# Kernel tuning notes

Measured on AMD Instinct MI355X. Metric: run time of the kernel, lower is better.

Reference implementation:

```python
import jax, jax.numpy as jnp
import numpy as np

K_CODES = 64
EPS_LN = 1e-5


def hamilton_product(p, q):
    # p, q: [..., D] with D = 4*Q, components ordered (r, i, j, k)
    Q = p.shape[-1] // 4
    pr, pi, pj, pk = (p[..., :Q], p[..., Q:2*Q], p[..., 2*Q:3*Q], p[..., 3*Q:])
    qr, qi, qj, qk = (q[..., :Q], q[..., Q:2*Q], q[..., 2*Q:3*Q], q[..., 3*Q:])
    out_r = pr * qr - pi * qi - pj * qj - pk * qk
    out_i = pr * qi + pi * qr + pj * qk - pk * qj
    out_j = pr * qj - pi * qk + pj * qr + pk * qi
    out_k = pr * qk + pi * qj - pj * qi + pk * qr
    return jnp.concatenate([out_r, out_i, out_j, out_k], axis=-1)


def quaternion_linear(x, w4, b):
    # w4: [4, Qo, Qi] stacked (r, i, j, k); builds Hamilton block matrix [D, D]
    r, i, j, k = w4[0], w4[1], w4[2], w4[3]
    W = jnp.block([[r, -i, -j, -k],
                   [i,  r, -k,  j],
                   [j,  k,  r, -i],
                   [k, -j,  i,  r]])
    return x @ W.T + b


def quaternion_layernorm(x, gamma, beta):
    # independent LayerNorm over each quaternion component (4 chunks of size Q)
    Qd = x.shape[-1] // 4
    xs = x.reshape(*x.shape[:-1], 4, Qd)
    mu = xs.mean(axis=-1, keepdims=True)
    var = ((xs - mu) ** 2).mean(axis=-1, keepdims=True)
    xn = (xs - mu) / jnp.sqrt(var + EPS_LN)
    out = xn * gamma + beta  # gamma/beta: [4, Qd]
    return out.reshape(*x.shape[:-1], 4 * Qd)


def setup_inputs() -> dict:
    key = jax.random.key(0)
    ks = jax.random.split(key, 8)
    B, N, D, m = 8, 4096, 512, 3
    Qd = D // 4
    q = jax.random.normal(ks[0], (B, N, D), dtype=jnp.float32)
    assign_idx = jax.random.randint(ks[1], (B, N, m), 0, K_CODES)
    assign_w = jax.random.uniform(ks[2], (B, N, m), dtype=jnp.float32)
    contribute_mask = jnp.ones((B, N), dtype=jnp.float32)
    scale = 0.5 / np.sqrt(Qd)
    proto_w = jax.random.normal(ks[3], (4, Qd, Qd), dtype=jnp.float32) * scale
    proto_b = jax.random.normal(ks[4], (D,), dtype=jnp.float32) * 0.01
    upd_w = jax.random.normal(ks[5], (4, Qd, Qd), dtype=jnp.float32) * scale
    upd_b = jax.random.normal(ks[6], (D,), dtype=jnp.float32) * 0.01
    ln_gamma = jnp.ones((4, Qd), dtype=jnp.float32)
    ln_beta = jnp.zeros((4, Qd), dtype=jnp.float32)
    return {"q": q, "assign_idx": assign_idx, "assign_w": assign_w,
            "contribute_mask": contribute_mask, "proto_w": proto_w,
            "proto_b": proto_b, "upd_w": upd_w, "upd_b": upd_b,
            "ln_gamma": ln_gamma, "ln_beta": ln_beta}


def reference(q, assign_idx, assign_w, contribute_mask, proto_w, proto_b,
              upd_w, upd_b, ln_gamma, ln_beta):
    B, N, D = q.shape
    m = assign_idx.shape[-1]
    K = K_CODES

    # --- scatter-add prototype aggregation ---
    agg_w = assign_w * contribute_mask[..., None]            # [B, N, m]
    flat_idx = assign_idx.reshape(B, N * m)                  # [B, N*m]
    flat_w = agg_w.reshape(B, N * m, 1)                      # [B, N*m, 1]
    weighted_q = (q[:, :, None, :] * agg_w[..., None]).reshape(B, N * m, D)

    seg = lambda v, idx: jax.ops.segment_sum(v, idx, num_segments=K)
    proto = jax.vmap(seg)(weighted_q, flat_idx)              # [B, K, D]
    weight_sum = jax.vmap(seg)(flat_w, flat_idx)             # [B, K, 1]
    proto = proto / (weight_sum + 1e-6)
    proto = quaternion_linear(proto, proto_w, proto_b)       # [B, K, D]

    # --- gather prototypes per observation + Hamilton routing ---
    proto_per_obs = jax.vmap(lambda p, idx: p[idx])(proto, assign_idx)  # [B, N, m, D]
    routed = hamilton_product(q[:, :, None, :], proto_per_obs)          # [B, N, m, D]
    msg = (routed * assign_w[..., None]).sum(axis=2)                    # [B, N, D]
    msg = quaternion_linear(msg, upd_w, upd_b)

    q_new = quaternion_layernorm(q + msg, ln_gamma, ln_beta)
    return q_new, proto
```

## Files before the change

### kernel.cpp

```cpp
#include <hip/hip_runtime.h>
#include <hip/hip_bf16.h>

#define B_ 8
#define N_ 4096
#define D_ 512
#define K_ 64
#define QD_ 128

typedef float f32x4 __attribute__((ext_vector_type(4)));
typedef short short8 __attribute__((ext_vector_type(8)));
typedef unsigned short u16;
typedef unsigned int u32;

__device__ __forceinline__ u16 f2bf(float f) {
  u32 u = __float_as_uint(f);
  return (u16)((u + 0x7fffu + ((u >> 16) & 1u)) >> 16);
}
__device__ __forceinline__ float bf2f(u16 h) {
  return __uint_as_float((u32)h << 16);
}

__device__ __forceinline__ void load8f(const float* p, float* r) {
  float4 a = *(const float4*)(p);
  float4 b = *(const float4*)(p + 4);
  r[0] = a.x; r[1] = a.y; r[2] = a.z; r[3] = a.w;
  r[4] = b.x; r[5] = b.y; r[6] = b.z; r[7] = b.w;
}

__global__ __launch_bounds__(256) void k_wexp_frag(
    const float* __restrict__ uw, const float* __restrict__ pw,
    u16* __restrict__ uwf, u16* __restrict__ pwf) {
  const int gid = blockIdx.x * 256 + threadIdx.x;
  const int sel = gid >> 18;
  const int idx = gid & ((1 << 18) - 1);
  const int e = idx & 7;
  const int lane = (idx >> 3) & 63;
  const int ks = (idx >> 9) & 15;
  const int cf = idx >> 13;
  const int col = (cf >> 3) * 128 + (cf & 7) * 16 + (lane & 15);
  const int v = ks * 32 + (lane >> 4) * 8 + e;
  const int u = col >> 7, a = col & 127, c = v >> 7, bb = v & 127;
  const int   matT[4][4] = {{0,1,2,3},{1,0,3,2},{2,3,0,1},{3,2,1,0}};
  const float sgnT[4][4] = {{1.f,-1.f,-1.f,-1.f},{1.f,1.f,-1.f,1.f},
                            {1.f,1.f,1.f,-1.f},{1.f,-1.f,1.f,1.f}};
  const float* w4 = sel ? pw : uw;
  u16* dst = sel ? pwf : uwf;
  dst[idx] = f2bf(sgnT[u][c] * w4[matT[u][c] * QD_ * QD_ + a * QD_ + bb]);
}

__global__ __launch_bounds__(256) void k_bldA(
    const int* __restrict__ aidx, const float* __restrict__ aw,
    const float* __restrict__ mask, u16* __restrict__ A) {
  const int gid = blockIdx.x * 256 + threadIdx.x;
  const int b = gid >> 12, n = gid & 4095;
  const size_t ib = (size_t)gid * 3;
  const int k0 = aidx[ib], k1 = aidx[ib + 1], k2 = aidx[ib + 2];
  const float mk = mask[gid];
  float w0 = aw[ib] * mk, w1 = aw[ib + 1] * mk, w2 = aw[ib + 2] * mk;
  bool skip1 = false, skip2 = false;
  if (k1 == k0) { w0 += w1; skip1 = true; }
  if (k2 == k0) { w0 += w2; skip2 = true; }
  else if (k2 == k1 && !skip1) { w1 += w2; skip2 = true; }
  u16* Ab = A + (size_t)b * K_ * N_;
  Ab[(size_t)k0 * N_ + n] = f2bf(w0);
  if (!skip1) Ab[(size_t)k1 * N_ + n] = f2bf(w1);
  if (!skip2) Ab[(size_t)k2 * N_ + n] = f2bf(w2);
}

__global__ __launch_bounds__(256) void k_gemmA(
    const u16* __restrict__ A, const float* __restrict__ q,
    float* __restrict__ proto_raw) {
  __shared__ __align__(16) u16 Bt[128 * 64];
  const int t = threadIdx.x;
  const int kc = blockIdx.x;
  const int dq = blockIdx.y;
  const int b = blockIdx.z;
  const int n_base = kc * 256;
  const u16* Ab = A + (size_t)b * K_ * N_;
  const float* qb = q + ((size_t)b * N_ + n_base) * D_ + dq * 128;

  const int lane = t & 63, wv = t >> 6;
  const int g = lane >> 4, l16 = lane & 15;
  const int sn = t >> 2, sdq = (t & 3) * 32;

  f32x4 acc[4][2];
#pragma unroll
  for (int mt = 0; mt < 4; ++mt)
#pragma unroll
    for (int nt = 0; nt < 2; ++nt) { f32x4 z = {0.f,0.f,0.f,0.f}; acc[mt][nt] = z; }

  float4 pre[8];
#pragma unroll
  for (int e = 0; e < 8; ++e)
    pre[e] = *(const float4*)(qb + (size_t)sn * D_ + sdq + e * 4);

  for (int sub = 0; sub < 4; ++sub) {
    __syncthreads();
#pragma unroll
    for (int e = 0; e < 8; ++e) {
      const float4 v = pre[e];
#pragma unroll
      for (int x = 0; x < 4; ++x) {
        const int d = sdq + e * 4 + x;
        const float fv = (x == 0) ? v.x : (x == 1) ? v.y : (x == 2) ? v.z : v.w;
        const int byte = (d * 128 + sn * 2) ^ ((d & 7) << 4);
        *(u16*)((char*)Bt + byte) = f2bf(fv);
      }
    }
    float4 nxt[8];
    if (sub < 3) {
#pragma unroll
      for (int e = 0; e < 8; ++e)
        nxt[e] = *(const float4*)(qb + (size_t)((sub + 1) * 64 + sn) * D_ + sdq + e * 4);
    }
    __syncthreads();
    const int n0 = n_base + sub * 64;
#pragma unroll
    for (int ks = 0; ks < 2; ++ks) {
      short8 bfrag[2];
#pragma unroll
      for (int nt = 0; nt < 2; ++nt) {
        const int d = wv * 32 + nt * 16 + l16;
        const int byte = (d * 128 + (ks * 32 + g * 8) * 2) ^ ((d & 7) << 4);
        bfrag[nt] = *(const short8*)((const char*)Bt + byte);
      }
#pragma unroll
      for (int mt = 0; mt < 4; ++mt) {
        const short8 afr = *(const short8*)(Ab + (size_t)(mt * 16 + l16) * N_ +
                                            n0 + ks * 32 + g * 8);
#pragma unroll
        for (int nt = 0; nt < 2; ++nt)
          acc[mt][nt] = __builtin_amdgcn_mfma_f32_16x16x32_bf16(afr, bfrag[nt], acc[mt][nt], 0, 0, 0);
      }
    }
#pragma unroll
    for (int e = 0; e < 8; ++e) pre[e] = nxt[e];
  }

#pragma unroll
  for (int mt = 0; mt < 4; ++mt)
#pragma unroll
    for (int nt = 0; nt < 2; ++nt)
#pragma unroll
      for (int rg = 0; rg < 4; ++rg) {
        const int code = mt * 16 + g * 4 + rg;
        const int d = dq * 128 + wv * 32 + nt * 16 + l16;
        atomicAdd(&proto_raw[((size_t)b * K_ + code) * D_ + d], acc[mt][nt][rg]);
      }
}

__global__ __launch_bounds__(64) void k_rowsum(const u16* __restrict__ A,
                                               float* __restrict__ wsum) {
  const int row = blockIdx.x;
  const int t = threadIdx.x;
  const u16* p = A + (size_t)row * N_ + t * 64;
  float s = 0.f;
#pragma unroll
  for (int i = 0; i < 8; ++i) {
    const short8 v = *(const short8*)(p + i * 8);
#pragma unroll
    for (int e = 0; e < 8; ++e) s += bf2f((u16)v[e]);
  }
  s += __shfl_xor(s, 1);  s += __shfl_xor(s, 2);  s += __shfl_xor(s, 4);
  s += __shfl_xor(s, 8);  s += __shfl_xor(s, 16); s += __shfl_xor(s, 32);
  if (t == 0) wsum[row] = s;
}

__global__ __launch_bounds__(256) void k_proto_mfma(
    const float* __restrict__ proto_raw, const float* __restrict__ wsum,
    const u16* __restrict__ pwf, const float* __restrict__ pb,
    float* __restrict__ proto_t, float* __restrict__ out_proto) {
  __shared__ __align__(16) u16 msgL[16 * 512];
  __shared__ float invs[16];
  const int t = threadIdx.x;
  const size_t R0 = (size_t)blockIdx.x * 16;
  if (t < 16) invs[t] = 1.f / (wsum[R0 + t] + 1e-6f);
  __syncthreads();

  {
    const int s = t & 15, row = t >> 4;
    const float iv = invs[row];
    const float* base = proto_raw + (R0 + row) * D_;
    const int swz = (row & 7) << 4;
#pragma unroll
    for (int u = 0; u < 4; ++u) {
      float m[8];
      load8f(base + u * 128 + s * 8, m);
      uint4 val;
      val.x = (u32)f2bf(m[0]*iv) | ((u32)f2bf(m[1]*iv) << 16);
      val.y = (u32)f2bf(m[2]*iv) | ((u32)f2bf(m[3]*iv) << 16);
      val.z = (u32)f2bf(m[4]*iv) | ((u32)f2bf(m[5]*iv) << 16);
      val.w = (u32)f2bf(m[6]*iv) | ((u32)f2bf(m[7]*iv) << 16);
      const int byte = (row * 1024 + u * 256 + s * 16) ^ swz;
      *(uint4*)((char*)msgL + byte) = val;
    }
  }
  __syncthreads();

  const int lane = t & 63, wv = t >> 6;
  const int g = lane >> 4, l16 = lane & 15;
  f32x4 acc[8];
#pragma unroll
  for (int f = 0; f < 8; ++f) { f32x4 z = {0.f,0.f,0.f,0.f}; acc[f] = z; }
#pragma unroll 4
  for (int ks = 0; ks < 16; ++ks) {
    const int arow = l16;
    const short8 a = *(const short8*)((const char*)msgL +
        ((arow * 1024 + ks * 64 + g * 16) ^ ((arow & 7) << 4)));
#pragma unroll
    for (int f = 0; f < 8; ++f) {
      const short8 bv = *(const short8*)(pwf +
          ((size_t)((wv * 8 + f) * 16 + ks) * 64 + lane) * 8);
      acc[f] = __builtin_amdgcn_mfma_f32_16x16x32_bf16(a, bv, acc[f], 0, 0, 0);
    }
  }

#pragma unroll
  for (int f = 0; f < 8; ++f) {
    const int col = wv * 128 + f * 16 + l16;
    const float pbv = pb[col];
#pragma unroll
    for (int rg = 0; rg < 4; ++rg) {
      const size_t row = R0 + g * 4 + rg;
      const float v = acc[f][rg] + pbv;
      proto_t[row * D_ + col] = v;
      out_proto[row * D_ + col] = v;
    }
  }
}

__global__ __launch_bounds__(256) void k_main7b(
    const float* __restrict__ q, const int* __restrict__ aidx,
    const float* __restrict__ aw, const float* __restrict__ proto_t,
    const u16* __restrict__ uwf, const float* __restrict__ ub,
    const float* __restrict__ gamma, const float* __restrict__ beta,
    float* __restrict__ out_q) {
  __shared__ __align__(16) u16 msgL[32 * 512];
  const int t = threadIdx.x;
  const size_t R0 = (size_t)blockIdx.x * 32;

  {
    const int s = t & 15, rowHalf = t >> 4;
    int kks[2][3]; float wws[2][3];
#pragma unroll
    for (int p = 0; p < 2; ++p) {
      const size_t gr = R0 + p * 16 + rowHalf;
      const int* ip = aidx + gr * 3;
      const float* wp = aw + gr * 3;
#pragma unroll
      for (int j = 0; j < 3; ++j) { kks[p][j] = ip[j]; wws[p][j] = wp[j]; }
    }
#pragma unroll
    for (int p = 0; p < 2; ++p) {
      const int row = p * 16 + rowHalf;
      const size_t gr = R0 + row;
      const int b = (int)(gr >> 12);
      const float* qp = q + gr * D_ + s * 8;
      float qr_[8], qi_[8], qj_[8], qk_[8];
      load8f(qp, qr_); load8f(qp + 128, qi_);
      load8f(qp + 256, qj_); load8f(qp + 384, qk_);
      float mr[8], mi[8], mj[8], mk[8];
#pragma unroll
      for (int e = 0; e < 8; ++e) { mr[e] = mi[e] = mj[e] = mk[e] = 0.f; }
#pragma unroll
      for (int j = 0; j < 3; ++j) {
        const float w = wws[p][j];
        const float* pp = proto_t + (size_t)(b * K_ + kks[p][j]) * D_ + s * 8;
        float pr[8], pi[8], pj[8], pk[8];
        load8f(pp, pr); load8f(pp + 128, pi);
        load8f(pp + 256, pj); load8f(pp + 384, pk);
#pragma unroll
        for (int e = 0; e < 8; ++e) {
          mr[e] += w * (qr_[e]*pr[e] - qi_[e]*pi[e] - qj_[e]*pj[e] - qk_[e]*pk[e]);
          mi[e] += w * (qr_[e]*pi[e] + qi_[e]*pr[e] + qj_[e]*pk[e] - qk_[e]*pj[e]);
          mj[e] += w * (qr_[e]*pj[e] - qi_[e]*pk[e] + qj_[e]*pr[e] + qk_[e]*pi[e]);
          mk[e] += w * (qr_[e]*pk[e] + qi_[e]*pj[e] - qj_[e]*pi[e] + qk_[e]*pr[e]);
        }
      }
      const int swz = (row & 7) << 4;
      const float* srcs[4] = {mr, mi, mj, mk};
#pragma unroll
      for (int u = 0; u < 4; ++u) {
        const float* m = srcs[u];
        uint4 val;
        val.x = (u32)f2bf(m[0]) | ((u32)f2bf(m[1]) << 16);
        val.y = (u32)f2bf(m[2]) | ((u32)f2bf(m[3]) << 16);
        val.z = (u32)f2bf(m[4]) | ((u32)f2bf(m[5]) << 16);
        val.w = (u32)f2bf(m[6]) | ((u32)f2bf(m[7]) << 16);
        const int byte = (row * 1024 + u * 256 + s * 16) ^ swz;
        *(uint4*)((char*)msgL + byte) = val;
      }
    }
  }
  __syncthreads();

  const int lane = t & 63, c4 = t >> 6;
  const int g = lane >> 4, l16 = lane & 15;
  f32x4 acc[2][8];
#pragma unroll
  for (int st = 0; st < 2; ++st)
#pragma unroll
    for (int f = 0; f < 8; ++f) { f32x4 z = {0.f,0.f,0.f,0.f}; acc[st][f] = z; }
#pragma unroll 2
  for (int ks = 0; ks < 16; ++ks) {
    short8 bfr[8];
#pragma unroll
    for (int f = 0; f < 8; ++f)
      bfr[f] = *(const short8*)(uwf +
          ((size_t)((c4 * 8 + f) * 16 + ks) * 64 + lane) * 8);
#pragma unroll
    for (int st = 0; st < 2; ++st) {
      const int arow = st * 16 + l16;
      const short8 a = *(const short8*)((const char*)msgL +
          ((arow * 1024 + ks * 64 + g * 16) ^ ((arow & 7) << 4)));
#pragma unroll
      for (int f = 0; f < 8; ++f)
        acc[st][f] = __builtin_amdgcn_mfma_f32_16x16x32_bf16(a, bfr[f], acc[st][f], 0, 0, 0);
    }
  }

  const int colQ = c4 * 128;
#pragma unroll
  for (int st = 0; st < 2; ++st)
#pragma unroll
    for (int f = 0; f < 8; ++f) {
      const int col = colQ + f * 16 + l16;
      const float ubv = ub[col];
#pragma unroll
      for (int rg = 0; rg < 4; ++rg) {
        const size_t row = R0 + st * 16 + g * 4 + rg;
        acc[st][f][rg] += ubv + q[row * D_ + col];
      }
    }
#pragma unroll
  for (int st = 0; st < 2; ++st)
#pragma unroll
    for (int rg = 0; rg < 4; ++rg) {
      float s = 0.f;
#pragma unroll
      for (int f = 0; f < 8; ++f) s += acc[st][f][rg];
      s += __shfl_xor(s, 1); s += __shfl_xor(s, 2);
      s += __shfl_xor(s, 4); s += __shfl_xor(s, 8);
      const float mean = s * 0.0078125f;
      float sq = 0.f;
#pragma unroll
      for (int f = 0; f < 8; ++f) {
        const float d = acc[st][f][rg] - mean; sq += d * d;
      }
      sq += __shfl_xor(sq, 1); sq += __shfl_xor(sq, 2);
      sq += __shfl_xor(sq, 4); sq += __shfl_xor(sq, 8);
      const float rstd = rsqrtf(sq * 0.0078125f + 1e-5f);
      const size_t row = R0 + st * 16 + g * 4 + rg;
#pragma unroll
      for (int f = 0; f < 8; ++f) {
        const int col = colQ + f * 16 + l16;
        const float xn = (acc[st][f][rg] - mean) * rstd;
        out_q[row * D_ + col] = xn * gamma[col] + beta[col];
      }
    }
}

extern "C" void kernel_launch(void* const* d_in, const int* in_sizes, int n_in,
                              void* d_out, int out_size, void* d_ws, size_t ws_size,
                              hipStream_t stream) {
  const float* q     = (const float*)d_in[0];
  const int*   aidx  = (const int*)d_in[1];
  const float* aw    = (const float*)d_in[2];
  const float* mask  = (const float*)d_in[3];
  const float* pw    = (const float*)d_in[4];
  const float* pb    = (const float*)d_in[5];
  const float* uw    = (const float*)d_in[6];
  const float* ub    = (const float*)d_in[7];
  const float* gamma = (const float*)d_in[8];
  const float* beta  = (const float*)d_in[9];

  char* ws = (char*)d_ws;
  const size_t MB = 1 << 20;
  float* proto_raw = (float*)ws;
  float* wsum      = (float*)(ws + MB);
  u16*   A         = (u16*)(ws + MB + 4096);
  float* proto_t   = (float*)(ws + 5 * MB + 4096);
  u16*   uwf       = (u16*)(ws + 6 * MB + 4096);
  u16*   pwf       = (u16*)(ws + 6 * MB + 4096 + (512 << 10));

  float* out_q = (float*)d_out;
  float* out_proto = out_q + (size_t)B_ * N_ * D_;

  hipMemsetAsync(ws, 0, 5 * MB + 4096, stream);
  k_wexp_frag<<<2048, 256, 0, stream>>>(uw, pw, uwf, pwf);
  k_bldA<<<128, 256, 0, stream>>>(aidx, aw, mask, A);
  k_gemmA<<<dim3(16, 4, 8), 256, 0, stream>>>(A, q, proto_raw);
  k_rowsum<<<512, 64, 0, stream>>>(A, wsum);
  k_proto_mfma<<<32, 256, 0, stream>>>(proto_raw, wsum, pwf, pb, proto_t, out_proto);
  k_main7b<<<1024, 256, 0, stream>>>(q, aidx, aw, proto_t, uwf, ub, gamma, beta, out_q);
}
```

Baseline: 138.3 us.

## Factor Hamilton product out of prototype sum, fuse rowsum into GEMM, zero A in-kernel

```diff
diff --git a/kernel.cpp b/kernel.cpp
--- a/kernel.cpp
+++ b/kernel.cpp
@@ -25,6 +25,17 @@
   float4 b = *(const float4*)(p + 4);
   r[0] = a.x; r[1] = a.y; r[2] = a.z; r[3] = a.w;
   r[4] = b.x; r[5] = b.y; r[6] = b.z; r[7] = b.w;
+}
+
+__device__ __forceinline__ void store_comp(char* msgL, int row, int u, int s,
+                                           int swz, const float* m) {
+  uint4 val;
+  val.x = (u32)f2bf(m[0]) | ((u32)f2bf(m[1]) << 16);
+  val.y = (u32)f2bf(m[2]) | ((u32)f2bf(m[3]) << 16);
+  val.z = (u32)f2bf(m[4]) | ((u32)f2bf(m[5]) << 16);
+  val.w = (u32)f2bf(m[6]) | ((u32)f2bf(m[7]) << 16);
+  const int byte = (row * 1024 + u * 256 + s * 16) ^ swz;
+  *(uint4*)(msgL + byte) = val;
 }
 
 __global__ __launch_bounds__(256) void k_wexp_frag(
@@ -62,6 +73,8 @@
   if (k2 == k0) { w0 += w2; skip2 = true; }
   else if (k2 == k1 && !skip1) { w1 += w2; skip2 = true; }
   u16* Ab = A + (size_t)b * K_ * N_;
+#pragma unroll
+  for (int k = 0; k < K_; ++k) Ab[(size_t)k * N_ + n] = 0;
   Ab[(size_t)k0 * N_ + n] = f2bf(w0);
   if (!skip1) Ab[(size_t)k1 * N_ + n] = f2bf(w1);
   if (!skip2) Ab[(size_t)k2 * N_ + n] = f2bf(w2);
@@ -69,7 +82,7 @@
 
 __global__ __launch_bounds__(256) void k_gemmA(
     const u16* __restrict__ A, const float* __restrict__ q,
-    float* __restrict__ proto_raw) {
+    float* __restrict__ proto_raw, float* __restrict__ wsum) {
   __shared__ __align__(16) u16 Bt[128 * 64];
   const int t = threadIdx.x;
   const int kc = blockIdx.x;
@@ -147,23 +160,21 @@
         const int d = dq * 128 + wv * 32 + nt * 16 + l16;
         atomicAdd(&proto_raw[((size_t)b * K_ + code) * D_ + d], acc[mt][nt][rg]);
       }
-}
-
-__global__ __launch_bounds__(64) void k_rowsum(const u16* __restrict__ A,
-                                               float* __restrict__ wsum) {
-  const int row = blockIdx.x;
-  const int t = threadIdx.x;
-  const u16* p = A + (size_t)row * N_ + t * 64;
-  float s = 0.f;
-#pragma unroll
-  for (int i = 0; i < 8; ++i) {
-    const short8 v = *(const short8*)(p + i * 8);
-#pragma unroll
-    for (int e = 0; e < 8; ++e) s += bf2f((u16)v[e]);
-  }
-  s += __shfl_xor(s, 1);  s += __shfl_xor(s, 2);  s += __shfl_xor(s, 4);
-  s += __shfl_xor(s, 8);  s += __shfl_xor(s, 16); s += __shfl_xor(s, 32);
-  if (t == 0) wsum[row] = s;
+
+  if (dq == 0) {
+    const int k = t >> 2, part = t & 3;
+    const u16* ap = Ab + (size_t)k * N_ + n_base + part * 64;
+    float s = 0.f;
+#pragma unroll
+    for (int i = 0; i < 8; ++i) {
+      const short8 v = *(const short8*)(ap + i * 8);
+#pragma unroll
+      for (int e = 0; e < 8; ++e) s += bf2f((u16)v[e]);
+    }
+    s += __shfl_xor(s, 1);
+    s += __shfl_xor(s, 2);
+    if (part == 0) atomicAdd(&wsum[b * K_ + k], s);
+  }
 }
 
 __global__ __launch_bounds__(256) void k_proto_mfma(
@@ -186,13 +197,9 @@
     for (int u = 0; u < 4; ++u) {
       float m[8];
       load8f(base + u * 128 + s * 8, m);
-      uint4 val;
-      val.x = (u32)f2bf(m[0]*iv) | ((u32)f2bf(m[1]*iv) << 16);
-      val.y = (u32)f2bf(m[2]*iv) | ((u32)f2bf(m[3]*iv) << 16);
-      val.z = (u32)f2bf(m[4]*iv) | ((u32)f2bf(m[5]*iv) << 16);
-      val.w = (u32)f2bf(m[6]*iv) | ((u32)f2bf(m[7]*iv) << 16);
-      const int byte = (row * 1024 + u * 256 + s * 16) ^ swz;
-      *(uint4*)((char*)msgL + byte) = val;
+#pragma unroll
+      for (int e = 0; e < 8; ++e) m[e] *= iv;
+      store_comp((char*)msgL, row, u, s, swz, m);
     }
   }
   __syncthreads();
@@ -229,7 +236,7 @@
   }
 }
 
-__global__ __launch_bounds__(256) void k_main7b(
+__global__ __launch_bounds__(256) void k_main8(
     const float* __restrict__ q, const int* __restrict__ aidx,
     const float* __restrict__ aw, const float* __restrict__ proto_t,
     const u16* __restrict__ uwf, const float* __restrict__ ub,
@@ -259,9 +266,9 @@
       float qr_[8], qi_[8], qj_[8], qk_[8];
       load8f(qp, qr_); load8f(qp + 128, qi_);
       load8f(qp + 256, qj_); load8f(qp + 384, qk_);
-      float mr[8], mi[8], mj[8], mk[8];
-#pragma unroll
-      for (int e = 0; e < 8; ++e) { mr[e] = mi[e] = mj[e] = mk[e] = 0.f; }
+      float Pr[8], Pi[8], Pj[8], Pk[8];
+#pragma unroll
+      for (int e = 0; e < 8; ++e) { Pr[e] = Pi[e] = Pj[e] = Pk[e] = 0.f; }
 #pragma unroll
       for (int j = 0; j < 3; ++j) {
         const float w = wws[p][j];
@@ -271,25 +278,28 @@
         load8f(pp + 256, pj); load8f(pp + 384, pk);
 #pragma unroll
         for (int e = 0; e < 8; ++e) {
-          mr[e] += w * (qr_[e]*pr[e] - qi_[e]*pi[e] - qj_[e]*pj[e] - qk_[e]*pk[e]);
-          mi[e] += w * (qr_[e]*pi[e] + qi_[e]*pr[e] + qj_[e]*pk[e] - qk_[e]*pj[e]);
-          mj[e] += w * (qr_[e]*pj[e] - qi_[e]*pk[e] + qj_[e]*pr[e] + qk_[e]*pi[e]);
-          mk[e] += w * (qr_[e]*pk[e] + qi_[e]*pj[e] - qj_[e]*pi[e] + qk_[e]*pr[e]);
+          Pr[e] += w * pr[e]; Pi[e] += w * pi[e];
+          Pj[e] += w * pj[e]; Pk[e] += w * pk[e];
         }
       }
       const int swz = (row & 7) << 4;
-      const float* srcs[4] = {mr, mi, mj, mk};
-#pragma unroll
-      for (int u = 0; u < 4; ++u) {
-        const float* m = srcs[u];
-        uint4 val;
-        val.x = (u32)f2bf(m[0]) | ((u32)f2bf(m[1]) << 16);
-        val.y = (u32)f2bf(m[2]) | ((u32)f2bf(m[3]) << 16);
-        val.z = (u32)f2bf(m[4]) | ((u32)f2bf(m[5]) << 16);
-        val.w = (u32)f2bf(m[6]) | ((u32)f2bf(m[7]) << 16);
-        const int byte = (row * 1024 + u * 256 + s * 16) ^ swz;
-        *(uint4*)((char*)msgL + byte) = val;
-      }
+      float m[8];
+#pragma unroll
+      for (int e = 0; e < 8; ++e)
+        m[e] = qr_[e]*Pr[e] - qi_[e]*Pi[e] - qj_[e]*Pj[e] - qk_[e]*Pk[e];
+      store_comp((char*)msgL, row, 0, s, swz, m);
+#pragma unroll
+      for (int e = 0; e < 8; ++e)
+        m[e] = qr_[e]*Pi[e] + qi_[e]*Pr[e] + qj_[e]*Pk[e] - qk_[e]*Pj[e];
+      store_comp((char*)msgL, row, 1, s, swz, m);
+#pragma unroll
+      for (int e = 0; e < 8; ++e)
+        m[e] = qr_[e]*Pj[e] - qi_[e]*Pk[e] + qj_[e]*Pr[e] + qk_[e]*Pi[e];
+      store_comp((char*)msgL, row, 2, s, swz, m);
+#pragma unroll
+      for (int e = 0; e < 8; ++e)
+        m[e] = qr_[e]*Pk[e] + qi_[e]*Pj[e] - qj_[e]*Pi[e] + qk_[e]*Pr[e];
+      store_comp((char*)msgL, row, 3, s, swz, m);
     }
   }
   __syncthreads();
@@ -386,11 +396,10 @@
   float* out_q = (float*)d_out;
   float* out_proto = out_q + (size_t)B_ * N_ * D_;
 
-  hipMemsetAsync(ws, 0, 5 * MB + 4096, stream);
+  hipMemsetAsync(ws, 0, MB + 4096, stream);
   k_wexp_frag<<<2048, 256, 0, stream>>>(uw, pw, uwf, pwf);
   k_bldA<<<128, 256, 0, stream>>>(aidx, aw, mask, A);
-  k_gemmA<<<dim3(16, 4, 8), 256, 0, stream>>>(A, q, proto_raw);
-  k_rowsum<<<512, 64, 0, stream>>>(A, wsum);
+  k_gemmA<<<dim3(16, 4, 8), 256, 0, stream>>>(A, q, proto_raw, wsum);
   k_proto_mfma<<<32, 256, 0, stream>>>(proto_raw, wsum, pwf, pb, proto_t, out_proto);
-  k_main7b<<<1024, 256, 0, stream>>>(q, aidx, aw, proto_t, uwf, ub, gamma, beta, out_q);
-}
+  k_main8<<<1024, 256, 0, stream>>>(q, aidx, aw, proto_t, uwf, ub, gamma, beta, out_q);
+}
```

After: 131.6 us. 1.05x faster.
